# Performance work log

Measured on AMD Instinct MI355X. Metric: run time of the kernel, lower is better.

The kernel has to match this reference:

```python
import jax, jax.numpy as jnp
import numpy as np

VOCAB, D_EMBED, D_HID = 32000, 512, 512
T, B, S = 64, 32, 256


def setup_inputs() -> dict:
    key = jax.random.key(0)
    ks = jax.random.split(key, 12)
    sE = 1.0 / np.sqrt(D_EMBED)
    sH = 1.0 / np.sqrt(D_HID)
    return {
        "x_seq": jax.random.randint(ks[0], (T, B), 0, VOCAB),
        "h": jax.random.normal(ks[1], (B, D_HID), jnp.float32),
        "c": jax.random.normal(ks[2], (B, D_HID), jnp.float32),
        "context": jax.random.normal(ks[3], (B, S, D_HID), jnp.float32),
        "emb": jax.random.normal(ks[4], (VOCAB, D_EMBED), jnp.float32),
        "W_ih": jax.random.normal(ks[5], (4 * D_HID, D_EMBED), jnp.float32) * sE,
        "W_hh": jax.random.normal(ks[6], (4 * D_HID, D_HID), jnp.float32) * sH,
        "b_ih": jax.random.normal(ks[7], (4 * D_HID,), jnp.float32) * sH,
        "b_hh": jax.random.normal(ks[8], (4 * D_HID,), jnp.float32) * sH,
        "W_attn": jax.random.normal(ks[9], (D_HID, 2 * D_HID), jnp.float32) * sH,
        "W_out": jax.random.normal(ks[10], (VOCAB, D_HID), jnp.float32) * sH,
        "b_out": jax.random.normal(ks[11], (VOCAB,), jnp.float32) * sH,
    }


def reference(x_seq, h, c, context, emb, W_ih, W_hh, b_ih, b_hh, W_attn, W_out, b_out):
    e_seq = emb[x_seq]  # [T, B, E]

    def step(carry, e):
        h, c = carry
        gates = e @ W_ih.T + b_ih + h @ W_hh.T + b_hh  # [B, 4H]
        i, f, g, o = jnp.split(gates, 4, axis=-1)       # torch LSTMCell gate order
        i, f, o = jax.nn.sigmoid(i), jax.nn.sigmoid(f), jax.nn.sigmoid(o)
        g = jnp.tanh(g)
        c = f * c + i * g
        h = o * jnp.tanh(c)
        # dot global attention
        scores = jnp.einsum('bsd,bd->bs', context, h)
        attn = jax.nn.softmax(scores, axis=1)
        wctx = jnp.einsum('bs,bsd->bd', attn, context)
        a = jnp.tanh(jnp.concatenate([h, wctx], axis=1) @ W_attn.T)
        return (h, c), a

    (hf, cf), outs = jax.lax.scan(step, (h, c), e_seq)  # outs: [T, B, H]
    logits = outs.reshape(-1, D_HID) @ W_out.T + b_out   # [T*B, V]
    logp = jax.nn.log_softmax(logits, axis=1).reshape(T, B, VOCAB)
    return logp, hf, cf
```

## Files before the change

kernel.cpp:

```cpp
#include <hip/hip_runtime.h>
#include <hip/hip_cooperative_groups.h>
#include <cstdint>
#include <cstddef>

namespace cg = cooperative_groups;

#define TT 64
#define BB 32
#define SS 256
#define DH 512
#define VV 32000
#define NROWS 2048
#define G4 2048
#define NBLK_SCAN 256
#define NLEAF 8
#define LEAF_TARGET (NBLK_SCAN / NLEAF)

typedef __attribute__((ext_vector_type(8))) short short8;
typedef __attribute__((ext_vector_type(4))) float f32x4;

__device__ __forceinline__ unsigned short f2bf(float x) {
    unsigned u = __float_as_uint(x);
    u += 0x7FFFu + ((u >> 16) & 1u);
    return (unsigned short)(u >> 16);
}

__device__ __forceinline__ void gload_lds16(const void* g, void* l) {
    __builtin_amdgcn_global_load_lds(
        (const __attribute__((address_space(1))) unsigned int*)g,
        (__attribute__((address_space(3))) unsigned int*)l, 16, 0, 0);
}

__device__ __forceinline__ void coh_store(float* p, float v) {
    __hip_atomic_store(p, v, __ATOMIC_RELAXED, __HIP_MEMORY_SCOPE_AGENT);
}

__global__ void k_convert_bf16(const float* __restrict__ src,
                               unsigned short* __restrict__ dst, int n4) {
    int i = blockIdx.x * blockDim.x + threadIdx.x;
    int stride = gridDim.x * blockDim.x;
    for (; i < n4; i += stride) {
        float4 v = ((const float4*)src)[i];
        ushort4 o;
        o.x = f2bf(v.x); o.y = f2bf(v.y); o.z = f2bf(v.z); o.w = f2bf(v.w);
        ((ushort4*)dst)[i] = o;
    }
}

__global__ void k_gather_embed32(const int* __restrict__ xseq,
                                 const float* __restrict__ emb,
                                 float* __restrict__ ef) {
    int r = blockIdx.x;
    int tok = xseq[r];
    const float4* s = (const float4*)(emb + (size_t)tok * DH);
    float4* d = (float4*)(ef + (size_t)r * DH);
    for (int i = threadIdx.x; i < DH / 4; i += blockDim.x) d[i] = s[i];
}

__global__ void k_scan_init(int* __restrict__ cnt) {
    int i = blockIdx.x * blockDim.x + threadIdx.x;
    if (i < TT * 128) cnt[i] = 0;
}

__global__ __launch_bounds__(256)
void k_sgemm_xpart(const float* __restrict__ A, const float* __restrict__ B,
                   const float* __restrict__ bias1, const float* __restrict__ bias2,
                   float* __restrict__ Ct, int M, int N, int K) {
    __shared__ float As[16][128];
    __shared__ float Bs[16][132];

    const int tid = threadIdx.x;
    const int tx = tid & 15, ty = tid >> 4;
    const int m0 = blockIdx.y * 128, n0 = blockIdx.x * 128;
    const int r = tid >> 1;
    const int c8 = (tid & 1) * 8;

    float acc[8][8] = {};

    for (int kt = 0; kt < K; kt += 16) {
        float4 a0 = *(const float4*)&A[(size_t)(m0 + r) * K + kt + c8];
        float4 a1 = *(const float4*)&A[(size_t)(m0 + r) * K + kt + c8 + 4];
        float4 b0 = *(const float4*)&B[(size_t)(n0 + r) * K + kt + c8];
        float4 b1 = *(const float4*)&B[(size_t)(n0 + r) * K + kt + c8 + 4];
        __syncthreads();
        As[c8 + 0][r] = a0.x; As[c8 + 1][r] = a0.y; As[c8 + 2][r] = a0.z; As[c8 + 3][r] = a0.w;
        As[c8 + 4][r] = a1.x; As[c8 + 5][r] = a1.y; As[c8 + 6][r] = a1.z; As[c8 + 7][r] = a1.w;
        Bs[c8 + 0][r] = b0.x; Bs[c8 + 1][r] = b0.y; Bs[c8 + 2][r] = b0.z; Bs[c8 + 3][r] = b0.w;
        Bs[c8 + 4][r] = b1.x; Bs[c8 + 5][r] = b1.y; Bs[c8 + 6][r] = b1.z; Bs[c8 + 7][r] = b1.w;
        __syncthreads();
#pragma unroll
        for (int kk = 0; kk < 16; ++kk) {
            float4 av0 = *(const float4*)&As[kk][ty * 8];
            float4 av1 = *(const float4*)&As[kk][ty * 8 + 4];
            float4 bv0 = *(const float4*)&Bs[kk][tx * 8];
            float4 bv1 = *(const float4*)&Bs[kk][tx * 8 + 4];
            float av[8] = {av0.x, av0.y, av0.z, av0.w, av1.x, av1.y, av1.z, av1.w};
            float bv[8] = {bv0.x, bv0.y, bv0.z, bv0.w, bv1.x, bv1.y, bv1.z, bv1.w};
#pragma unroll
            for (int i = 0; i < 8; ++i)
#pragma unroll
                for (int j = 0; j < 8; ++j)
                    acc[i][j] += av[i] * bv[j];
        }
    }
#pragma unroll
    for (int i = 0; i < 8; ++i) {
        int grow = m0 + ty * 8 + i;
#pragma unroll
        for (int j = 0; j < 8; ++j) {
            int col = n0 + tx * 8 + j;
            Ct[(size_t)col * M + grow] = acc[i][j] + bias1[col] + bias2[col];
        }
    }
}

template <int EPI>
__global__ __launch_bounds__(256)
void k_mfma_gemm(const unsigned short* __restrict__ A,
                 const unsigned short* __restrict__ B,
                 int M, int N, int K,
                 const float* __restrict__ bias,
                 float* __restrict__ Cf,
                 unsigned short* __restrict__ Cbf,
                 float* __restrict__ pm, float* __restrict__ ps) {
    __shared__ unsigned short A_s[128 * 64];
    __shared__ unsigned short B_s[128 * 64];
    __shared__ float part_m[2][128];
    __shared__ float part_s[2][128];

    const int tid = threadIdx.x;
    const int lane = tid & 63;
    const int wid = tid >> 6;
    const int wm = wid >> 1, wn = wid & 1;
    const int mrow0 = blockIdx.y * 128;
    const int ncol0 = blockIdx.x * 128;
    const int lr = lane & 15;
    const int lk = (lane >> 4) * 8;
    const int rw = (lane >> 4) * 4;

    f32x4 acc[4][4] = {};

    for (int kt = 0; kt < K; kt += 64) {
#pragma unroll
        for (int it = 0; it < 4; ++it) {
            int chunk = it * 256 + tid;
            int r = chunk >> 3;
            int c = (chunk & 7) * 8;
            gload_lds16(A + (size_t)(mrow0 + r) * K + kt + c, (void*)(A_s + chunk * 8));
            gload_lds16(B + (size_t)(ncol0 + r) * K + kt + c, (void*)(B_s + chunk * 8));
        }
        __syncthreads();
#pragma unroll
        for (int kk = 0; kk < 2; ++kk) {
            short8 afr[4], bfr[4];
#pragma unroll
            for (int i = 0; i < 4; ++i) {
                afr[i] = *(const short8*)&A_s[(wm * 64 + i * 16 + lr) * 64 + kk * 32 + lk];
                bfr[i] = *(const short8*)&B_s[(wn * 64 + i * 16 + lr) * 64 + kk * 32 + lk];
            }
#pragma unroll
            for (int mi = 0; mi < 4; ++mi)
#pragma unroll
                for (int ni = 0; ni < 4; ++ni)
                    acc[mi][ni] = __builtin_amdgcn_mfma_f32_16x16x32_bf16(
                        afr[mi], bfr[ni], acc[mi][ni], 0, 0, 0);
        }
        __syncthreads();
    }

    if constexpr (EPI == 1) {
#pragma unroll
        for (int ni = 0; ni < 4; ++ni) {
            int col = ncol0 + wn * 64 + ni * 16 + lr;
#pragma unroll
            for (int mi = 0; mi < 4; ++mi)
#pragma unroll
                for (int r = 0; r < 4; ++r) {
                    int grow = mrow0 + wm * 64 + mi * 16 + rw + r;
                    Cbf[(size_t)grow * N + col] = f2bf(tanhf(acc[mi][ni][r]));
                }
        }
    } else {
        float bv[4];
#pragma unroll
        for (int ni = 0; ni < 4; ++ni) bv[ni] = bias[ncol0 + wn * 64 + ni * 16 + lr];
#pragma unroll
        for (int mi = 0; mi < 4; ++mi) {
#pragma unroll
            for (int r = 0; r < 4; ++r) {
                int grow = mrow0 + wm * 64 + mi * 16 + rw + r;
                float v[4];
                float mx = -1e30f;
#pragma unroll
                for (int ni = 0; ni < 4; ++ni) {
                    v[ni] = acc[mi][ni][r] + bv[ni];
                    int col = ncol0 + wn * 64 + ni * 16 + lr;
                    Cf[(size_t)grow * N + col] = v[ni];
                    mx = fmaxf(mx, v[ni]);
                }
#pragma unroll
                for (int d = 1; d <= 8; d <<= 1) mx = fmaxf(mx, __shfl_xor(mx, d));
                float ssum = 0.f;
#pragma unroll
                for (int ni = 0; ni < 4; ++ni) ssum += __expf(v[ni] - mx);
#pragma unroll
                for (int d = 1; d <= 8; d <<= 1) ssum += __shfl_xor(ssum, d);
                if (lr == 0) {
                    int lrow = wm * 64 + mi * 16 + rw + r;
                    part_m[wn][lrow] = mx;
                    part_s[wn][lrow] = ssum;
                }
            }
        }
        __syncthreads();
        if (tid < 128) {
            float m0v = part_m[0][tid], m1v = part_m[1][tid];
            float mm = fmaxf(m0v, m1v);
            float ssum = part_s[0][tid] * __expf(m0v - mm) + part_s[1][tid] * __expf(m1v - mm);
            int grow = mrow0 + tid;
            pm[(size_t)grow * gridDim.x + blockIdx.x] = mm;
            ps[(size_t)grow * gridDim.x + blockIdx.x] = ssum;
        }
    }
}

__global__ __launch_bounds__(512, 2)
void k_lstm_scan(const float* __restrict__ xpartT, const float* __restrict__ Whh,
                 const float* __restrict__ h0, const float* __restrict__ c0,
                 float* __restrict__ hTA, float* __restrict__ hTB,
                 float* __restrict__ Hall, unsigned short* __restrict__ catbuf,
                 float* __restrict__ hf, float* __restrict__ cf,
                 int* __restrict__ cnt) {
    __shared__ __align__(16) float h_lds[BB * 8 * 17 * 4];

    const int tid = threadIdx.x;
    const int jl = tid >> 8;
    const int bq = (tid >> 4) & 15;
    const int ks = tid & 15;
    const int jj = blockIdx.x * 2 + jl;

    f32x4 wreg[4][8];
#pragma unroll
    for (int g = 0; g < 4; ++g) {
        const float* wp = Whh + (size_t)(g * DH + jj) * DH + ks * 32;
#pragma unroll
        for (int r = 0; r < 8; ++r)
            wreg[g][r] = *(const f32x4*)(wp + r * 4);
    }

    float creg0 = c0[(size_t)bq * DH + jj];
    float creg1 = c0[(size_t)(bq + 16) * DH + jj];

    for (int t = 0; t < TT; ++t) {
        float xg0a = 0.f, xg1a = 0.f, xg2a = 0.f, xg3a = 0.f;
        float xg0b = 0.f, xg1b = 0.f, xg2b = 0.f, xg3b = 0.f;
        if (ks == 0) {
            const float* xt = xpartT + (size_t)t * BB;
            xg0a = xt[(size_t)(0 * DH + jj) * NROWS + bq];
            xg1a = xt[(size_t)(1 * DH + jj) * NROWS + bq];
            xg2a = xt[(size_t)(2 * DH + jj) * NROWS + bq];
            xg3a = xt[(size_t)(3 * DH + jj) * NROWS + bq];
            xg0b = xt[(size_t)(0 * DH + jj) * NROWS + bq + 16];
            xg1b = xt[(size_t)(1 * DH + jj) * NROWS + bq + 16];
            xg2b = xt[(size_t)(2 * DH + jj) * NROWS + bq + 16];
            xg3b = xt[(size_t)(3 * DH + jj) * NROWS + bq + 16];
        }

        const float* hR = (t == 0) ? h0 : ((t & 1) ? hTA : hTB);
        {
            f32x4 v[8];
#pragma unroll
            for (int q = 0; q < 8; ++q)
                asm volatile("global_load_dwordx4 %0, %1, off sc0 sc1"
                             : "=&v"(v[q]) : "v"(hR + (q * 512 + tid) * 4));
            asm volatile("s_waitcnt vmcnt(0)" ::: "memory");
            __builtin_amdgcn_sched_barrier(0);
#pragma unroll
            for (int q = 0; q < 8; ++q) {
                int f = q * 512 + tid;
                int b2 = f >> 7;
                int ks2 = (f & 127) >> 3;
                int r2 = f & 7;
                *(f32x4*)&h_lds[((b2 * 8 + r2) * 17 + ks2) * 4] = v[q];
            }
        }
        __syncthreads();

        float a0a = 0.f, a1a = 0.f, a2a = 0.f, a3a = 0.f;
        float a0b = 0.f, a1b = 0.f, a2b = 0.f, a3b = 0.f;
#pragma unroll
        for (int r = 0; r < 8; ++r) {
            f32x4 ha = *(const f32x4*)&h_lds[((bq * 8 + r) * 17 + ks) * 4];
            f32x4 hb = *(const f32x4*)&h_lds[(((bq + 16) * 8 + r) * 17 + ks) * 4];
            a0a += wreg[0][r][0] * ha[0] + wreg[0][r][1] * ha[1]
                 + wreg[0][r][2] * ha[2] + wreg[0][r][3] * ha[3];
            a1a += wreg[1][r][0] * ha[0] + wreg[1][r][1] * ha[1]
                 + wreg[1][r][2] * ha[2] + wreg[1][r][3] * ha[3];
            a2a += wreg[2][r][0] * ha[0] + wreg[2][r][1] * ha[1]
                 + wreg[2][r][2] * ha[2] + wreg[2][r][3] * ha[3];
            a3a += wreg[3][r][0] * ha[0] + wreg[3][r][1] * ha[1]
                 + wreg[3][r][2] * ha[2] + wreg[3][r][3] * ha[3];
            a0b += wreg[0][r][0] * hb[0] + wreg[0][r][1] * hb[1]
                 + wreg[0][r][2] * hb[2] + wreg[0][r][3] * hb[3];
            a1b += wreg[1][r][0] * hb[0] + wreg[1][r][1] * hb[1]
                 + wreg[1][r][2] * hb[2] + wreg[1][r][3] * hb[3];
            a2b += wreg[2][r][0] * hb[0] + wreg[2][r][1] * hb[1]
                 + wreg[2][r][2] * hb[2] + wreg[2][r][3] * hb[3];
            a3b += wreg[3][r][0] * hb[0] + wreg[3][r][1] * hb[1]
                 + wreg[3][r][2] * hb[2] + wreg[3][r][3] * hb[3];
        }
#pragma unroll
        for (int d = 1; d <= 8; d <<= 1) {
            a0a += __shfl_xor(a0a, d); a1a += __shfl_xor(a1a, d);
            a2a += __shfl_xor(a2a, d); a3a += __shfl_xor(a3a, d);
            a0b += __shfl_xor(a0b, d); a1b += __shfl_xor(a1b, d);
            a2b += __shfl_xor(a2b, d); a3b += __shfl_xor(a3b, d);
        }

        if (ks == 0) {
            float* wb = (t & 1) ? hTB : hTA;
#pragma unroll
            for (int bh = 0; bh < 2; ++bh) {
                int b = bh ? bq + 16 : bq;
                float gi = (bh ? a0b : a0a) + (bh ? xg0b : xg0a);
                float gf = (bh ? a1b : a1a) + (bh ? xg1b : xg1a);
                float gg = (bh ? a2b : a2a) + (bh ? xg2b : xg2a);
                float go = (bh ? a3b : a3a) + (bh ? xg3b : xg3a);
                float si = 1.f / (1.f + __expf(-gi));
                float sf = 1.f / (1.f + __expf(-gf));
                float tg = tanhf(gg);
                float so = 1.f / (1.f + __expf(-go));
                float cc = bh ? creg1 : creg0;
                cc = sf * cc + si * tg;
                float hn = so * tanhf(cc);
                if (bh) creg1 = cc; else creg0 = cc;

                coh_store(&wb[(size_t)b * DH + jj], hn);
                int row = t * BB + b;
                Hall[(size_t)row * DH + jj] = hn;
                catbuf[(size_t)row * 1024 + jj] = f2bf(hn);
                if (t == TT - 1) {
                    hf[(size_t)b * DH + jj] = hn;
                    cf[(size_t)b * DH + jj] = cc;
                }
            }
        }

        __syncthreads();
        if (tid == 0) {
            asm volatile("s_waitcnt vmcnt(0)" ::: "memory");
            __hip_atomic_fetch_add(&cnt[t * 128 + (blockIdx.x & (NLEAF - 1)) * 16], 1,
                                   __ATOMIC_RELAXED, __HIP_MEMORY_SCOPE_AGENT);
        }
        if (tid < NLEAF) {
            while (__hip_atomic_load(&cnt[t * 128 + tid * 16], __ATOMIC_RELAXED,
                                     __HIP_MEMORY_SCOPE_AGENT) < LEAF_TARGET) {
                __builtin_amdgcn_s_sleep(1);
            }
        }
        __syncthreads();
    }
}

__global__ __launch_bounds__(256)
void k_attn(const float* __restrict__ Hall, const float* __restrict__ ctx,
            unsigned short* __restrict__ catbuf) {
    __shared__ float h4[4][DH];
    __shared__ float p_lds[4][SS];
    __shared__ float l_lds[4];

    const int tid = threadIdx.x;
    const int b = blockIdx.x & 31;
    const int tg = blockIdx.x >> 5;

    for (int i = tid; i < 4 * DH / 4; i += 256) {
        int e = i * 4;
        int ti = e >> 9, k = e & 511;
        float4 v = *(const float4*)(Hall + ((size_t)((tg * 4 + ti) * BB + b)) * DH + k);
        h4[ti][k + 0] = v.x; h4[ti][k + 1] = v.y; h4[ti][k + 2] = v.z; h4[ti][k + 3] = v.w;
    }
    __syncthreads();

    {
        int s = tid;
        float acc[4] = {0.f, 0.f, 0.f, 0.f};
        const float4* cp = (const float4*)(ctx + ((size_t)b * SS + s) * DH);
        for (int kc = 0; kc < DH / 4; ++kc) {
            float4 cv = cp[kc];
#pragma unroll
            for (int i = 0; i < 4; ++i) {
                float4 hv = *(const float4*)&h4[i][kc * 4];
                acc[i] += cv.x * hv.x + cv.y * hv.y + cv.z * hv.z + cv.w * hv.w;
            }
        }
#pragma unroll
        for (int i = 0; i < 4; ++i) p_lds[i][s] = acc[i];
    }
    __syncthreads();

    {
        int w = tid >> 6, l = tid & 63;
        float v0 = p_lds[w][l], v1 = p_lds[w][l + 64];
        float v2 = p_lds[w][l + 128], v3 = p_lds[w][l + 192];
        float mx = fmaxf(fmaxf(v0, v1), fmaxf(v2, v3));
        for (int d = 1; d < 64; d <<= 1) mx = fmaxf(mx, __shfl_xor(mx, d));
        float e0 = __expf(v0 - mx), e1 = __expf(v1 - mx);
        float e2 = __expf(v2 - mx), e3 = __expf(v3 - mx);
        float ssum = e0 + e1 + e2 + e3;
        for (int d = 1; d < 64; d <<= 1) ssum += __shfl_xor(ssum, d);
        p_lds[w][l] = e0; p_lds[w][l + 64] = e1;
        p_lds[w][l + 128] = e2; p_lds[w][l + 192] = e3;
        if (l == 0) l_lds[w] = ssum;
    }
    __syncthreads();

    {
        int d0 = tid * 2;
        float accx[4], accy[4];
#pragma unroll
        for (int i = 0; i < 4; ++i) { accx[i] = 0.f; accy[i] = 0.f; }
        const float* cb = ctx + (size_t)b * SS * DH + d0;
        for (int s = 0; s < SS; ++s) {
            float2 cv = *(const float2*)(cb + (size_t)s * DH);
#pragma unroll
            for (int i = 0; i < 4; ++i) {
                float p = p_lds[i][s];
                accx[i] += p * cv.x;
                accy[i] += p * cv.y;
            }
        }
#pragma unroll
        for (int i = 0; i < 4; ++i) {
            float inv = 1.f / l_lds[i];
            int row = (tg * 4 + i) * BB + b;
            unsigned pack = (unsigned)f2bf(accx[i] * inv) | ((unsigned)f2bf(accy[i] * inv) << 16);
            *(unsigned*)&catbuf[(size_t)row * 1024 + DH + d0] = pack;
        }
    }
}

__global__ __launch_bounds__(256)
void k_lsesub(float* __restrict__ logp, const float* __restrict__ pm,
              const float* __restrict__ ps, int nt) {
    __shared__ float sL;
    const int row = blockIdx.x;
    const int tid = threadIdx.x;
    if (tid < 64) {
        const float* pmr = pm + (size_t)row * nt;
        const float* psr = ps + (size_t)row * nt;
        float m = -1e30f;
        for (int i = tid; i < nt; i += 64) m = fmaxf(m, pmr[i]);
        for (int d = 1; d < 64; d <<= 1) m = fmaxf(m, __shfl_xor(m, d));
        float s = 0.f;
        for (int i = tid; i < nt; i += 64) s += psr[i] * __expf(pmr[i] - m);
        for (int d = 1; d < 64; d <<= 1) s += __shfl_xor(s, d);
        if (tid == 0) sL = m + logf(s);
    }
    __syncthreads();
    float L = sL;
    float4* p = (float4*)(logp + (size_t)row * VV);
    for (int i = tid; i < VV / 4; i += 256) {
        float4 v = p[i];
        v.x -= L; v.y -= L; v.z -= L; v.w -= L;
        p[i] = v;
    }
}

extern "C" void kernel_launch(void* const* d_in, const int* in_sizes, int n_in,
                              void* d_out, int out_size, void* d_ws, size_t ws_size,
                              hipStream_t stream) {
    const int*   xseq  = (const int*)d_in[0];
    const float* h0    = (const float*)d_in[1];
    const float* c0    = (const float*)d_in[2];
    const float* ctx   = (const float*)d_in[3];
    const float* emb   = (const float*)d_in[4];
    const float* Wih   = (const float*)d_in[5];
    const float* Whh   = (const float*)d_in[6];
    const float* bih   = (const float*)d_in[7];
    const float* bhh   = (const float*)d_in[8];
    const float* Wattn = (const float*)d_in[9];
    const float* Wout  = (const float*)d_in[10];
    const float* bout  = (const float*)d_in[11];
    float* out = (float*)d_out;

    char* wptr = (char*)d_ws;
    auto carve = [&](size_t bytes) {
        char* p = wptr;
        wptr += (bytes + 255) & ~(size_t)255;
        return p;
    };
    float*          xpartT  = (float*)carve((size_t)NROWS * G4 * 4);
    float*          Hall    = (float*)carve((size_t)NROWS * DH * 4);
    unsigned short* catbf   = (unsigned short*)carve((size_t)NROWS * 1024 * 2);
    unsigned short* outsbf  = (unsigned short*)carve((size_t)NROWS * DH * 2);
    float*          ef32    = (float*)carve((size_t)NROWS * DH * 4);
    unsigned short* Wattnbf = (unsigned short*)carve((size_t)DH * 1024 * 2);
    unsigned short* Woutbf  = (unsigned short*)carve((size_t)VV * DH * 2);
    float*          hTA     = (float*)carve((size_t)BB * DH * 4);
    float*          hTB     = (float*)carve((size_t)BB * DH * 4);
    int*            cnt     = (int*)carve((size_t)TT * 128 * 4);
    float*          pm      = (float*)carve((size_t)NROWS * 250 * 4);
    float*          ps      = (float*)carve((size_t)NROWS * 250 * 4);

    k_convert_bf16<<<256, 256, 0, stream>>>(Wattn, Wattnbf, DH * 1024 / 4);
    k_convert_bf16<<<2048, 256, 0, stream>>>(Wout, Woutbf, VV * DH / 4);
    k_gather_embed32<<<NROWS, 128, 0, stream>>>(xseq, emb, ef32);
    k_scan_init<<<32, 256, 0, stream>>>(cnt);

    k_sgemm_xpart<<<dim3(16, 16), 256, 0, stream>>>(
        ef32, Wih, bih, bhh, xpartT, NROWS, G4, DH);

    {
        const float* a0 = xpartT; const float* a1 = Whh;
        const float* a2 = h0;     const float* a3 = c0;
        float* a4 = hTA; float* a5 = hTB; float* a6 = Hall;
        unsigned short* a7 = catbf;
        float* a8 = out + (size_t)NROWS * VV;
        float* a9 = a8 + BB * DH;
        int* a10 = cnt;
        void* args[] = {&a0, &a1, &a2, &a3, &a4, &a5, &a6, &a7, &a8, &a9, &a10};
        hipLaunchCooperativeKernel((const void*)k_lstm_scan, dim3(NBLK_SCAN), dim3(512),
                                   args, 0, stream);
    }

    k_attn<<<512, 256, 0, stream>>>(Hall, ctx, catbf);

    k_mfma_gemm<1><<<dim3(4, 16), 256, 0, stream>>>(
        catbf, Wattnbf, NROWS, DH, 1024, nullptr, nullptr, outsbf, nullptr, nullptr);

    k_mfma_gemm<2><<<dim3(250, 16), 256, 0, stream>>>(
        outsbf, Woutbf, NROWS, VV, DH, bout, out, nullptr, pm, ps);

    k_lsesub<<<NROWS, 256, 0, stream>>>(out, pm, ps, 250);
}
```

Before: 982.2 us.

## Replace FP32 SIMT input-projection GEMM with split-bf16 MFMA and widen barrier leaves

The input-projection GEMM (embeddings times W_ih) now runs on bf16 MFMA instead of the FP32 register-tiled SGEMM. To keep near-FP32 accuracy, each operand is split into high and low bf16 parts, and three MFMA products (hi*hi, hi*lo, lo*hi) are accumulated. This adds conversion kernels for W_ih and the gathered embeddings, plus extra memory traffic for the hi/lo buffers. Separately, the scan's grid barrier uses 32 leaf counters instead of 8 to reduce atomic contention per counter, at the cost of more counters for each waiting thread to poll.

```diff
diff --git a/kernel.cpp b/kernel.cpp
--- a/kernel.cpp
+++ b/kernel.cpp
@@ -13,7 +13,7 @@
 #define NROWS 2048
 #define G4 2048
 #define NBLK_SCAN 256
-#define NLEAF 8
+#define NLEAF 32
 #define LEAF_TARGET (NBLK_SCAN / NLEAF)
 
 typedef __attribute__((ext_vector_type(8))) short short8;
@@ -23,6 +23,9 @@
     unsigned u = __float_as_uint(x);
     u += 0x7FFFu + ((u >> 16) & 1u);
     return (unsigned short)(u >> 16);
+}
+__device__ __forceinline__ float bf2f(unsigned short u) {
+    return __uint_as_float((unsigned)u << 16);
 }
 
 __device__ __forceinline__ void gload_lds16(const void* g, void* l) {
@@ -47,69 +50,133 @@
     }
 }
 
-__global__ void k_gather_embed32(const int* __restrict__ xseq,
-                                 const float* __restrict__ emb,
-                                 float* __restrict__ ef) {
+__global__ void k_convert_hl(const float* __restrict__ src,
+                             unsigned short* __restrict__ hi,
+                             unsigned short* __restrict__ lo, int n4) {
+    int i = blockIdx.x * blockDim.x + threadIdx.x;
+    int stride = gridDim.x * blockDim.x;
+    for (; i < n4; i += stride) {
+        float4 v = ((const float4*)src)[i];
+        ushort4 oh, ol;
+        float f[4] = {v.x, v.y, v.z, v.w};
+        unsigned short h[4], l[4];
+#pragma unroll
+        for (int e = 0; e < 4; ++e) {
+            h[e] = f2bf(f[e]);
+            l[e] = f2bf(f[e] - bf2f(h[e]));
+        }
+        oh.x = h[0]; oh.y = h[1]; oh.z = h[2]; oh.w = h[3];
+        ol.x = l[0]; ol.y = l[1]; ol.z = l[2]; ol.w = l[3];
+        ((ushort4*)hi)[i] = oh;
+        ((ushort4*)lo)[i] = ol;
+    }
+}
+
+__global__ void k_gather_embed_hl(const int* __restrict__ xseq,
+                                  const float* __restrict__ emb,
+                                  unsigned short* __restrict__ ehi,
+                                  unsigned short* __restrict__ elo) {
     int r = blockIdx.x;
     int tok = xseq[r];
     const float4* s = (const float4*)(emb + (size_t)tok * DH);
-    float4* d = (float4*)(ef + (size_t)r * DH);
-    for (int i = threadIdx.x; i < DH / 4; i += blockDim.x) d[i] = s[i];
+    ushort4* dh = (ushort4*)(ehi + (size_t)r * DH);
+    ushort4* dl = (ushort4*)(elo + (size_t)r * DH);
+    for (int i = threadIdx.x; i < DH / 4; i += blockDim.x) {
+        float4 v = s[i];
+        float f[4] = {v.x, v.y, v.z, v.w};
+        unsigned short h[4], l[4];
+#pragma unroll
+        for (int e = 0; e < 4; ++e) {
+            h[e] = f2bf(f[e]);
+            l[e] = f2bf(f[e] - bf2f(h[e]));
+        }
+        dh[i] = make_ushort4(h[0], h[1], h[2], h[3]);
+        dl[i] = make_ushort4(l[0], l[1], l[2], l[3]);
+    }
 }
 
 __global__ void k_scan_init(int* __restrict__ cnt) {
     int i = blockIdx.x * blockDim.x + threadIdx.x;
-    if (i < TT * 128) cnt[i] = 0;
+    if (i < TT * NLEAF * 16) cnt[i] = 0;
 }
 
 __global__ __launch_bounds__(256)
-void k_sgemm_xpart(const float* __restrict__ A, const float* __restrict__ B,
-                   const float* __restrict__ bias1, const float* __restrict__ bias2,
-                   float* __restrict__ Ct, int M, int N, int K) {
-    __shared__ float As[16][128];
-    __shared__ float Bs[16][132];
+void k_mfma_xpart(const unsigned short* __restrict__ Ahi, const unsigned short* __restrict__ Alo,
+                  const unsigned short* __restrict__ Bhi, const unsigned short* __restrict__ Blo,
+                  int M, int N, int K,
+                  const float* __restrict__ b1, const float* __restrict__ b2,
+                  float* __restrict__ Ct) {
+    __shared__ unsigned short Ah_s[128 * 64];
+    __shared__ unsigned short Al_s[128 * 64];
+    __shared__ unsigned short Bh_s[128 * 64];
+    __shared__ unsigned short Bl_s[128 * 64];
 
     const int tid = threadIdx.x;
-    const int tx = tid & 15, ty = tid >> 4;
-    const int m0 = blockIdx.y * 128, n0 = blockIdx.x * 128;
-    const int r = tid >> 1;
-    const int c8 = (tid & 1) * 8;
-
-    float acc[8][8] = {};
-
-    for (int kt = 0; kt < K; kt += 16) {
-        float4 a0 = *(const float4*)&A[(size_t)(m0 + r) * K + kt + c8];
-        float4 a1 = *(const float4*)&A[(size_t)(m0 + r) * K + kt + c8 + 4];
-        float4 b0 = *(const float4*)&B[(size_t)(n0 + r) * K + kt + c8];
-        float4 b1 = *(const float4*)&B[(size_t)(n0 + r) * K + kt + c8 + 4];
-        __syncthreads();
-        As[c8 + 0][r] = a0.x; As[c8 + 1][r] = a0.y; As[c8 + 2][r] = a0.z; As[c8 + 3][r] = a0.w;
-        As[c8 + 4][r] = a1.x; As[c8 + 5][r] = a1.y; As[c8 + 6][r] = a1.z; As[c8 + 7][r] = a1.w;
-        Bs[c8 + 0][r] = b0.x; Bs[c8 + 1][r] = b0.y; Bs[c8 + 2][r] = b0.z; Bs[c8 + 3][r] = b0.w;
-        Bs[c8 + 4][r] = b1.x; Bs[c8 + 5][r] = b1.y; Bs[c8 + 6][r] = b1.z; Bs[c8 + 7][r] = b1.w;
-        __syncthreads();
-#pragma unroll
-        for (int kk = 0; kk < 16; ++kk) {
-            float4 av0 = *(const float4*)&As[kk][ty * 8];
-            float4 av1 = *(const float4*)&As[kk][ty * 8 + 4];
-            float4 bv0 = *(const float4*)&Bs[kk][tx * 8];
-            float4 bv1 = *(const float4*)&Bs[kk][tx * 8 + 4];
-            float av[8] = {av0.x, av0.y, av0.z, av0.w, av1.x, av1.y, av1.z, av1.w};
-            float bv[8] = {bv0.x, bv0.y, bv0.z, bv0.w, bv1.x, bv1.y, bv1.z, bv1.w};
-#pragma unroll
-            for (int i = 0; i < 8; ++i)
-#pragma unroll
-                for (int j = 0; j < 8; ++j)
-                    acc[i][j] += av[i] * bv[j];
-        }
-    }
-#pragma unroll
-    for (int i = 0; i < 8; ++i) {
-        int grow = m0 + ty * 8 + i;
-#pragma unroll
-        for (int j = 0; j < 8; ++j) {
-            int col = n0 + tx * 8 + j;
-            Ct[(size_t)col * M + grow] = acc[i][j] + bias1[col] + bias2[col];
+    const int lane = tid & 63;
+    const int wid = tid >> 6;
+    const int wm = wid >> 1, wn = wid & 1;
+    const int mrow0 = blockIdx.y * 128;
+    const int ncol0 = blockIdx.x * 128;
+    const int lr = lane & 15;
+    const int lk = (lane >> 4) * 8;
+    const int rw = (lane >> 4) * 4;
+
+    f32x4 acc[4][4] = {};
+
+    for (int kt = 0; kt < K; kt += 64) {
+#pragma unroll
+        for (int it = 0; it < 4; ++it) {
+            int chunk = it * 256 + tid;
+            int r = chunk >> 3;
+            int c = (chunk & 7) * 8;
+            size_t goA = (size_t)(mrow0 + r) * K + kt + c;
+            size_t goB = (size_t)(ncol0 + r) * K + kt + c;
+            gload_lds16(Ahi + goA, (void*)(Ah_s + chunk * 8));
+            gload_lds16(Alo + goA, (void*)(Al_s + chunk * 8));
+            gload_lds16(Bhi + goB, (void*)(Bh_s + chunk * 8));
+            gload_lds16(Blo + goB, (void*)(Bl_s + chunk * 8));
+        }
+        __syncthreads();
+#pragma unroll
+        for (int kk = 0; kk < 2; ++kk) {
+            short8 ah[4], al[4], bh[4], bl[4];
+#pragma unroll
+            for (int i = 0; i < 4; ++i) {
+                int offA = (wm * 64 + i * 16 + lr) * 64 + kk * 32 + lk;
+                int offB = (wn * 64 + i * 16 + lr) * 64 + kk * 32 + lk;
+                ah[i] = *(const short8*)&Ah_s[offA];
+                al[i] = *(const short8*)&Al_s[offA];
+                bh[i] = *(const short8*)&Bh_s[offB];
+                bl[i] = *(const short8*)&Bl_s[offB];
+            }
+#pragma unroll
+            for (int mi = 0; mi < 4; ++mi)
+#pragma unroll
+                for (int ni = 0; ni < 4; ++ni) {
+                    acc[mi][ni] = __builtin_amdgcn_mfma_f32_16x16x32_bf16(
+                        ah[mi], bh[ni], acc[mi][ni], 0, 0, 0);
+                    acc[mi][ni] = __builtin_amdgcn_mfma_f32_16x16x32_bf16(
+                        ah[mi], bl[ni], acc[mi][ni], 0, 0, 0);
+                    acc[mi][ni] = __builtin_amdgcn_mfma_f32_16x16x32_bf16(
+                        al[mi], bh[ni], acc[mi][ni], 0, 0, 0);
+                }
+        }
+        __syncthreads();
+    }
+
+#pragma unroll
+    for (int ni = 0; ni < 4; ++ni) {
+        int col = ncol0 + wn * 64 + ni * 16 + lr;
+        float bs = b1[col] + b2[col];
+#pragma unroll
+        for (int mi = 0; mi < 4; ++mi) {
+            int grow0 = mrow0 + wm * 64 + mi * 16 + rw;
+            float4 o;
+            o.x = acc[mi][ni][0] + bs;
+            o.y = acc[mi][ni][1] + bs;
+            o.z = acc[mi][ni][2] + bs;
+            o.w = acc[mi][ni][3] + bs;
+            *(float4*)&Ct[(size_t)col * M + grow0] = o;
         }
     }
 }
@@ -349,11 +416,11 @@
         __syncthreads();
         if (tid == 0) {
             asm volatile("s_waitcnt vmcnt(0)" ::: "memory");
-            __hip_atomic_fetch_add(&cnt[t * 128 + (blockIdx.x & (NLEAF - 1)) * 16], 1,
+            __hip_atomic_fetch_add(&cnt[t * (NLEAF * 16) + (blockIdx.x & (NLEAF - 1)) * 16], 1,
                                    __ATOMIC_RELAXED, __HIP_MEMORY_SCOPE_AGENT);
         }
         if (tid < NLEAF) {
-            while (__hip_atomic_load(&cnt[t * 128 + tid * 16], __ATOMIC_RELAXED,
+            while (__hip_atomic_load(&cnt[t * (NLEAF * 16) + tid * 16], __ATOMIC_RELAXED,
                                      __HIP_MEMORY_SCOPE_AGENT) < LEAF_TARGET) {
                 __builtin_amdgcn_s_sleep(1);
             }
@@ -493,22 +560,26 @@
     float*          Hall    = (float*)carve((size_t)NROWS * DH * 4);
     unsigned short* catbf   = (unsigned short*)carve((size_t)NROWS * 1024 * 2);
     unsigned short* outsbf  = (unsigned short*)carve((size_t)NROWS * DH * 2);
-    float*          ef32    = (float*)carve((size_t)NROWS * DH * 4);
+    unsigned short* ehi     = (unsigned short*)carve((size_t)NROWS * DH * 2);
+    unsigned short* elo     = (unsigned short*)carve((size_t)NROWS * DH * 2);
+    unsigned short* Wihhi   = (unsigned short*)carve((size_t)G4 * DH * 2);
+    unsigned short* Wihlo   = (unsigned short*)carve((size_t)G4 * DH * 2);
     unsigned short* Wattnbf = (unsigned short*)carve((size_t)DH * 1024 * 2);
     unsigned short* Woutbf  = (unsigned short*)carve((size_t)VV * DH * 2);
     float*          hTA     = (float*)carve((size_t)BB * DH * 4);
     float*          hTB     = (float*)carve((size_t)BB * DH * 4);
-    int*            cnt     = (int*)carve((size_t)TT * 128 * 4);
+    int*            cnt     = (int*)carve((size_t)TT * NLEAF * 16 * 4);
     float*          pm      = (float*)carve((size_t)NROWS * 250 * 4);
     float*          ps      = (float*)carve((size_t)NROWS * 250 * 4);
 
     k_convert_bf16<<<256, 256, 0, stream>>>(Wattn, Wattnbf, DH * 1024 / 4);
     k_convert_bf16<<<2048, 256, 0, stream>>>(Wout, Woutbf, VV * DH / 4);
-    k_gather_embed32<<<NROWS, 128, 0, stream>>>(xseq, emb, ef32);
-    k_scan_init<<<32, 256, 0, stream>>>(cnt);
-
-    k_sgemm_xpart<<<dim3(16, 16), 256, 0, stream>>>(
-        ef32, Wih, bih, bhh, xpartT, NROWS, G4, DH);
+    k_convert_hl<<<512, 256, 0, stream>>>(Wih, Wihhi, Wihlo, G4 * DH / 4);
+    k_gather_embed_hl<<<NROWS, 128, 0, stream>>>(xseq, emb, ehi, elo);
+    k_scan_init<<<128, 256, 0, stream>>>(cnt);
+
+    k_mfma_xpart<<<dim3(16, 16), 256, 0, stream>>>(
+        ehi, elo, Wihhi, Wihlo, NROWS, G4, DH, bih, bhh, xpartT);
 
     {
         const float* a0 = xpartT; const float* a1 = Whh;
```

After: 883.7 us. 1.11x faster.
